# Kernel tuning notes

Hardware: AMD Instinct MI355X
Metric: run time of the kernel (lower is better)

## Reference

```python
import jax, jax.numpy as jnp
import numpy as np

N, P, H, K = 8192, 32, 512, 100
D = 2 * P
R = 32  # min(32, max(8, H))


def setup_inputs() -> dict:
    key = jax.random.key(0)
    ks = jax.random.split(key, 12)
    # strictly increasing event times
    dts = jax.random.uniform(ks[0], (N,), dtype=jnp.float32) * 0.1 + 1e-3
    times = jnp.cumsum(dts)
    marks = jax.random.randint(ks[1], (N,), 0, K, dtype=jnp.int32)
    u_inputs = jax.random.normal(ks[2], (N, H), dtype=jnp.float32) * 0.1
    # parameters (match torch init scales)
    lambda_log_real = jax.random.normal(ks[3], (P,), dtype=jnp.float32) * 0.1
    lambda_im = jax.random.normal(ks[4], (P,), dtype=jnp.float32) * 0.05
    V = jnp.eye(D, dtype=jnp.float32) + 0.01 * jax.random.normal(ks[5], (D, D), dtype=jnp.float32)
    B = jax.random.normal(ks[6], (D, H), dtype=jnp.float32) * 0.05
    E = jax.random.normal(ks[7], (D, R), dtype=jnp.float32) * 0.05
    alpha = jax.random.normal(ks[8], (R, K), dtype=jnp.float32) * 0.05
    gate_w = jax.random.normal(ks[9], (P, H), dtype=jnp.float32) * 0.02
    gate_b = jax.random.normal(ks[10], (P,), dtype=jnp.float32) * 0.02
    x0 = jnp.zeros((D,), dtype=jnp.float32)
    return {"times": times, "marks": marks, "u_inputs": u_inputs,
            "lambda_log_real": lambda_log_real, "lambda_im": lambda_im,
            "V": V, "B": B, "E": E, "alpha": alpha,
            "gate_w": gate_w, "gate_b": gate_b, "x0": x0}


def _v_block(V, pr, pi):
    """V @ blockdiag_p([[pr,-pi],[pi,pr]]) for each step n. V:(D,D), pr/pi:(n,P) -> (n,D,D)."""
    Dd = V.shape[0]
    Pp = pr.shape[-1]
    Vr = V.reshape(Dd, Pp, 2)
    col0 = Vr[None, :, :, 0] * pr[:, None, :] + Vr[None, :, :, 1] * pi[:, None, :]
    col1 = -Vr[None, :, :, 0] * pi[:, None, :] + Vr[None, :, :, 1] * pr[:, None, :]
    return jnp.stack([col0, col1], axis=-1).reshape(-1, Dd, Dd)


def reference(times, marks, u_inputs, lambda_log_real, lambda_im, V, B, E, alpha, gate_w, gate_b, x0):
    n = times.shape[0]
    dt = jnp.concatenate([times[:1], jnp.diff(times)])  # (N,) t_0 - 0, t_i - t_{i-1}
    # input-dependent eigenvalues: real = -softplus(log_real) * softplus(Wu+b), imag fixed
    gate = jax.nn.softplus(u_inputs @ gate_w.T + gate_b)           # (N,P)
    real = -jax.nn.softplus(lambda_log_real)[None, :] * gate        # (N,P)
    imag = jnp.broadcast_to(lambda_im[None, :], real.shape)         # (N,P)
    dtc = dt[:, None]
    exps = jnp.exp(real * dtc)
    cosb = jnp.cos(imag * dtc)
    sinb = jnp.sin(imag * dtc)
    a = exps * cosb  # Re(exp(lam dt))
    c = exps * sinb  # Im(exp(lam dt))
    V_inv = jnp.linalg.inv(V)
    # exp(A dt) = V M V^{-1}, M block-rotation per mode
    Aexp = _v_block(V, a, c) @ V_inv                                # (N,D,D)
    # integral (exp(lam dt) - 1)/lam, with dt fallback near lam=0
    denom = real * real + imag * imag
    num_re = a - 1.0
    num_im = c
    qr = (num_re * real + num_im * imag) / (denom + 1e-12)
    qi = (num_im * real - num_re * imag) / (denom + 1e-12)
    small = denom < 1e-8
    qr = jnp.where(small, dtc, qr)
    qi = jnp.where(small, 0.0, qi)
    VMint = _v_block(V, qr, qi)                                     # (N,D,D)
    # cont = V M_int V^{-1} B u  (fuse V^{-1} B u first, avoiding Kmat materialization)
    w = u_inputs @ (V_inv @ B).T                                    # (N,D)
    cont = jnp.einsum('nij,nj->ni', VMint, w)
    cont = jnp.where(dtc > 0, cont, 0.0)
    # mark impulses r_k = E alpha[:, k]
    r = (E @ alpha)[:, marks].T                                     # (N,D)

    def step(x_prev, inp):
        A_i, c_i, r_i = inp
        x_left = A_i @ x_prev + c_i
        x_right = x_left + r_i
        return x_right, (x_right, x_left)

    _, (x_right, x_left) = jax.lax.scan(step, x0, (Aexp, cont, r))
    return x_right, x_left
```

## Files before the change

### kernel.cpp

```cpp
#include <hip/hip_runtime.h>
#include <math.h>

#define NN 8192
#define PP 32
#define HH 512
#define KK 100
#define DD 64
#define RR 32
#define MM 96
#define SB 32
#define NSEG 256

#define OFF_VINV 0
#define OFF_EAT  4096
#define OFF_RHT  10496
#define OFF_Y0   16896
#define OFF_BAGG 16960
#define OFF_C    49728
#define OFF_COEF 836160

__device__ __forceinline__ float sp_fast(float x) {
    return x > 15.f ? x : __logf(1.f + __expf(x));
}
__device__ __forceinline__ float rcp_fast(float x) {
    float r;
    asm("v_rcp_f32 %0, %1" : "=v"(r) : "v"(x));
    return r;
}
__device__ __forceinline__ float4 comp_aff(float4 f, float4 g) {
    float4 r;
    r.x = f.x * g.x - f.y * g.y;
    r.y = f.x * g.y + f.y * g.x;
    r.z = f.x * g.z - f.y * g.w + f.z;
    r.w = f.x * g.w + f.y * g.z + f.w;
    return r;
}

#define IDX(r,c) ((r)*64 + ((c) ^ (((r)&7)<<2)))

__global__ void __launch_bounds__(512) g0(
    const float* __restrict__ u, const float* __restrict__ gate_w,
    const float* __restrict__ B, const float* __restrict__ V,
    const float* __restrict__ E, const float* __restrict__ alpha,
    const float* __restrict__ x0, float* __restrict__ ws) {
    __shared__ float sm[16384];
    const int b = blockIdx.x, t = threadIdx.x;

    if (b == NSEG) {
        float* Vt = sm;
        float* X  = sm + 4096;
        float* Xt = sm + 8192;
        float* T  = sm + 12288;
        const int i0 = (t >> 4) << 1;
        const int j0 = (t & 15) << 2;
        float nx[2][4];
        #pragma unroll
        for (int r = 0; r < 2; r++) {
            float4 v4 = *(const float4*)&V[(i0 + r) * DD + j0];
            float vv[4] = {v4.x, v4.y, v4.z, v4.w};
            #pragma unroll
            for (int s = 0; s < 4; s++) {
                Vt[IDX(j0 + s, i0 + r)] = vv[s];
                float xv = ((i0 + r) == (j0 + s) ? 2.f : 0.f) - vv[s];
                nx[r][s] = xv;
                Xt[IDX(j0 + s, i0 + r)] = xv;
            }
            *(float4*)&X[IDX(i0 + r, j0)] =
                make_float4(nx[r][0], nx[r][1], nx[r][2], nx[r][3]);
        }
        __syncthreads();
        for (int it = 0; it < 2; it++) {
            float ac[2][4];
            #pragma unroll
            for (int r = 0; r < 2; r++)
                #pragma unroll
                for (int s = 0; s < 4; s++) ac[r][s] = 0.f;
            for (int k = 0; k < DD; k++) {
                float2 a2 = *(float2*)&Vt[IDX(k, i0)];
                float4 b4 = *(float4*)&X[IDX(k, j0)];
                float bv[4] = {b4.x, b4.y, b4.z, b4.w};
                #pragma unroll
                for (int s = 0; s < 4; s++) {
                    ac[0][s] = fmaf(a2.x, bv[s], ac[0][s]);
                    ac[1][s] = fmaf(a2.y, bv[s], ac[1][s]);
                }
            }
            #pragma unroll
            for (int r = 0; r < 2; r++)
                *(float4*)&T[IDX(i0 + r, j0)] =
                    make_float4(ac[r][0], ac[r][1], ac[r][2], ac[r][3]);
            __syncthreads();
            #pragma unroll
            for (int r = 0; r < 2; r++)
                #pragma unroll
                for (int s = 0; s < 4; s++) ac[r][s] = 0.f;
            for (int k = 0; k < DD; k++) {
                float2 a2 = *(float2*)&Xt[IDX(k, i0)];
                float4 b4 = *(float4*)&T[IDX(k, j0)];
                float bv[4] = {b4.x, b4.y, b4.z, b4.w};
                #pragma unroll
                for (int s = 0; s < 4; s++) {
                    ac[0][s] = fmaf(a2.x, bv[s], ac[0][s]);
                    ac[1][s] = fmaf(a2.y, bv[s], ac[1][s]);
                }
            }
            #pragma unroll
            for (int r = 0; r < 2; r++) {
                float4 xo = *(float4*)&X[IDX(i0 + r, j0)];
                nx[r][0] = 2.f * xo.x - ac[r][0];
                nx[r][1] = 2.f * xo.y - ac[r][1];
                nx[r][2] = 2.f * xo.z - ac[r][2];
                nx[r][3] = 2.f * xo.w - ac[r][3];
            }
            __syncthreads();
            #pragma unroll
            for (int r = 0; r < 2; r++) {
                *(float4*)&X[IDX(i0 + r, j0)] =
                    make_float4(nx[r][0], nx[r][1], nx[r][2], nx[r][3]);
                #pragma unroll
                for (int s = 0; s < 4; s++) Xt[IDX(j0 + s, i0 + r)] = nx[r][s];
            }
            __syncthreads();
        }
        #pragma unroll
        for (int r = 0; r < 2; r++)
            *(float4*)&ws[OFF_VINV + (i0 + r) * DD + j0] =
                make_float4(nx[r][0], nx[r][1], nx[r][2], nx[r][3]);
        for (int idx = t; idx < KK * DD; idx += 512) {
            int k = idx >> 6, d = idx & 63;
            float ea = 0.f;
            #pragma unroll
            for (int r = 0; r < RR; r++)
                ea = fmaf(E[d * RR + r], alpha[r * KK + k], ea);
            ws[OFF_EAT + idx] = ea;
            if (k < 64) Vt[k * 64 + d] = ea; else T[(k - 64) * 64 + d] = ea;
        }
        __syncthreads();
        for (int idx = t; idx < KK * DD; idx += 512) {
            int k = idx >> 6, d = idx & 63;
            const float* ea = (k < 64) ? &Vt[k * 64] : &T[(k - 64) * 64];
            float rr = 0.f;
            for (int j = 0; j < DD; j++) rr = fmaf(Xt[IDX(j, d)], ea[j], rr);
            ws[OFF_RHT + idx] = rr;
        }
        if (t < DD) {
            float s = 0.f;
            for (int j = 0; j < DD; j++) s = fmaf(Xt[IDX(j, t)], x0[j], s);
            ws[OFF_Y0 + t] = s;
        }
        return;
    }

    float* uT = sm;
    float* mT = sm + 2048;
    const int n0 = b * SB;
    const int tn = t & 15, tm = t >> 4;
    float acc0 = 0.f, acc1 = 0.f, acc2 = 0.f, acc3 = 0.f, acc4 = 0.f, acc5 = 0.f;
    for (int kc = 0; kc < HH; kc += 64) {
        {
            int r = t >> 4, c4 = t & 15;
            float4 f4 = *(const float4*)&u[(n0 + r) * HH + kc + c4 * 4];
            *(float4*)&uT[r * 64 + ((c4 ^ (r & 7)) << 2)] = f4;
        }
        #pragma unroll
        for (int s2 = 0; s2 < 3; s2++) {
            int idx = t + 512 * s2;
            int r = idx >> 4, c4 = idx & 15;
            const float* src = (r < 32) ? &gate_w[r * HH] : &B[(r - 32) * HH];
            float4 f4 = *(const float4*)&src[kc + c4 * 4];
            *(float4*)&mT[r * 64 + ((c4 ^ (r & 7)) << 2)] = f4;
        }
        __syncthreads();
        #pragma unroll
        for (int k4 = 0; k4 < 16; k4++) {
            float4 uu[2], mm[3];
            #pragma unroll
            for (int i = 0; i < 2; i++) {
                int rr = 2 * tn + i;
                uu[i] = *(float4*)&uT[rr * 64 + ((k4 ^ (rr & 7)) << 2)];
            }
            #pragma unroll
            for (int j = 0; j < 3; j++) {
                int m = 3 * tm + j;
                mm[j] = *(float4*)&mT[m * 64 + ((k4 ^ (m & 7)) << 2)];
            }
            acc0 += uu[0].x*mm[0].x + uu[0].y*mm[0].y + uu[0].z*mm[0].z + uu[0].w*mm[0].w;
            acc1 += uu[0].x*mm[1].x + uu[0].y*mm[1].y + uu[0].z*mm[1].z + uu[0].w*mm[1].w;
            acc2 += uu[0].x*mm[2].x + uu[0].y*mm[2].y + uu[0].z*mm[2].z + uu[0].w*mm[2].w;
            acc3 += uu[1].x*mm[0].x + uu[1].y*mm[0].y + uu[1].z*mm[0].z + uu[1].w*mm[0].w;
            acc4 += uu[1].x*mm[1].x + uu[1].y*mm[1].y + uu[1].z*mm[1].z + uu[1].w*mm[1].w;
            acc5 += uu[1].x*mm[2].x + uu[1].y*mm[2].y + uu[1].z*mm[2].z + uu[1].w*mm[2].w;
        }
        __syncthreads();
    }
    float* Cw = ws + OFF_C + (size_t)b * SB * MM;
    Cw[(2*tn+0) * MM + 3*tm+0] = acc0;
    Cw[(2*tn+0) * MM + 3*tm+1] = acc1;
    Cw[(2*tn+0) * MM + 3*tm+2] = acc2;
    Cw[(2*tn+1) * MM + 3*tm+0] = acc3;
    Cw[(2*tn+1) * MM + 3*tm+1] = acc4;
    Cw[(2*tn+1) * MM + 3*tm+2] = acc5;
}

__global__ void __launch_bounds__(512) g1(
    const float* __restrict__ times, const int* __restrict__ marks,
    const float* __restrict__ llr, const float* __restrict__ lim,
    const float* __restrict__ gate_b, float* __restrict__ ws) {
    __shared__ float sm[9600];
    const int b = blockIdx.x, t = threadIdx.x;
    const int n0 = b * SB;
    for (int idx = t; idx < DD * DD; idx += 512) {
        int d = idx >> 6, j = idx & 63;
        sm[j * 68 + d] = ws[OFF_VINV + idx];
    }
    {
        int r = t >> 4, c0 = (t & 15) * 6;
        const float* Cg = ws + OFF_C + (size_t)b * SB * MM + r * MM + c0;
        float* Cl = sm + 4352 + r * 100 + c0;
        #pragma unroll
        for (int q = 0; q < 3; q++)
            *(float2*)&Cl[2 * q] = *(const float2*)&Cg[2 * q];
    }
    __syncthreads();
    {
        const int nl = t >> 4, d0 = (t & 15) << 2;
        float4 a = {0.f, 0.f, 0.f, 0.f};
        for (int j = 0; j < DD; j++) {
            float cr = sm[4352 + nl * 100 + 32 + j];
            float4 v4 = *(float4*)&sm[j * 68 + d0];
            a.x = fmaf(cr, v4.x, a.x); a.y = fmaf(cr, v4.y, a.y);
            a.z = fmaf(cr, v4.z, a.z); a.w = fmaf(cr, v4.w, a.w);
        }
        __syncthreads();
        *(float4*)&sm[4352 + nl * 100 + 32 + d0] = a;
    }
    __syncthreads();
    const int c = t >> 5, p = t & 31;
    const float nlr = -sp_fast(llr[p]);
    const float imag = lim[p], gb = gate_b[p];
    float4 cfs[2];
    #pragma unroll
    for (int i = 0; i < 2; i++) {
        int nl = c * 2 + i, n = n0 + nl;
        float dtv = times[n] - (n ? times[n - 1] : 0.f);
        float gate = sp_fast(sm[4352 + nl * 100 + p] + gb);
        float real = nlr * gate;
        float e = __expf(real * dtv);
        float x = imag * dtv, x2 = x * x;
        float cb = 1.f - x2 * (0.5f - x2 * (1.f / 24.f));
        float sb = x * (1.f - x2 * ((1.f / 6.f) - x2 * (1.f / 120.f)));
        float a = e * cb, cc = e * sb;
        float denom = real * real + imag * imag;
        float inv = rcp_fast(denom + 1e-12f);
        float nre = a - 1.f, nim = cc;
        float qr = (nre * real + nim * imag) * inv;
        float qi = (nim * real - nre * imag) * inv;
        if (denom < 1e-8f) { qr = dtv; qi = 0.f; }
        float2 w = *(float2*)&sm[4352 + nl * 100 + 32 + 2 * p];
        float br = qr * w.x - qi * w.y;
        float bi = qr * w.y + qi * w.x;
        if (!(dtv > 0.f)) { br = 0.f; bi = 0.f; }
        int mk = marks[n];
        float2 rh = *(const float2*)&ws[OFF_RHT + mk * DD + 2 * p];
        cfs[i] = make_float4(a, cc, br + rh.x, bi + rh.y);
        *(float4*)&ws[OFF_COEF + ((size_t)n * PP + p) * 4] = cfs[i];
    }
    float4* ag = (float4*)(sm + 7552);
    ag[c * 32 + p] = comp_aff(cfs[1], cfs[0]);
    __syncthreads();
    if (t < PP) {
        float4 T = make_float4(1.f, 0.f, 0.f, 0.f);
        #pragma unroll
        for (int cc = 0; cc < 16; cc++) T = comp_aff(ag[cc * 32 + t], T);
        *(float4*)&ws[OFF_BAGG + (b * PP + t) * 4] = T;
    }
}

__global__ void __launch_bounds__(512) g2(
    const float* __restrict__ V, const int* __restrict__ marks,
    const float* __restrict__ ws, float* __restrict__ out) {
    __shared__ float sm[10688];
    const int b = blockIdx.x, t = threadIdx.x;
    const int n0 = b * SB;
    const int c = t >> 5, p = t & 31;
    for (int idx = t; idx < DD * DD; idx += 512) {
        int d = idx >> 6, k = idx & 63;
        sm[k * 68 + d] = V[idx];
    }
    float4 cf0 = *(const float4*)&ws[OFF_COEF + ((size_t)(n0 + c * 2)     * PP + p) * 4];
    float4 cf1 = *(const float4*)&ws[OFF_COEF + ((size_t)(n0 + c * 2 + 1) * PP + p) * 4];
    float4* ag   = (float4*)(sm + 4352);
    float4* pref = (float4*)(sm + 6400);
    float2* yb   = (float2*)(sm + 10624);
    ag[c * 32 + p] = comp_aff(cf1, cf0);
    {
        int q0 = c * 16, q1 = min(b, q0 + 16);
        float4 Q = make_float4(1.f, 0.f, 0.f, 0.f);
        for (int q = q0; q < q1; q++)
            Q = comp_aff(*(const float4*)&ws[OFF_BAGG + (q * PP + p) * 4], Q);
        pref[c * 32 + p] = Q;
    }
    __syncthreads();
    if (t < PP) {
        float2 y = *(const float2*)&ws[OFF_Y0 + 2 * t];
        #pragma unroll
        for (int jg = 0; jg < 16; jg++) {
            float4 Q = pref[jg * 32 + t];
            float nyr = Q.x * y.x - Q.y * y.y + Q.z;
            float nyi = Q.x * y.y + Q.y * y.x + Q.w;
            y.x = nyr; y.y = nyi;
        }
        yb[t] = y;
    }
    __syncthreads();
    {
        float2 y = yb[p];
        #pragma unroll
        for (int cc = 0; cc < 15; cc++) {
            if (cc < c) {
                float4 A = ag[cc * 32 + p];
                float nyr = A.x * y.x - A.y * y.y + A.z;
                float nyi = A.x * y.y + A.y * y.x + A.w;
                y.x = nyr; y.y = nyi;
            }
        }
        float nyr = cf0.x * y.x - cf0.y * y.y + cf0.z;
        float nyi = cf0.x * y.y + cf0.y * y.x + cf0.w;
        y.x = nyr; y.y = nyi;
        *(float2*)&sm[8448 + (c * 2 + 0) * 68 + 2 * p] = y;
        nyr = cf1.x * y.x - cf1.y * y.y + cf1.z;
        nyi = cf1.x * y.y + cf1.y * y.x + cf1.w;
        y.x = nyr; y.y = nyi;
        *(float2*)&sm[8448 + (c * 2 + 1) * 68 + 2 * p] = y;
    }
    __syncthreads();
    {
        const int nr = t >> 4, d0 = (t & 15) << 2;
        float4 a = {0.f, 0.f, 0.f, 0.f};
        for (int k = 0; k < DD; k++) {
            float yv = sm[8448 + nr * 68 + k];
            float4 v4 = *(float4*)&sm[k * 68 + d0];
            a.x = fmaf(yv, v4.x, a.x); a.y = fmaf(yv, v4.y, a.y);
            a.z = fmaf(yv, v4.z, a.z); a.w = fmaf(yv, v4.w, a.w);
        }
        int n = n0 + nr;
        int mk = marks[n];
        *(float4*)&out[(size_t)n * DD + d0] = a;
        float4 e4 = *(const float4*)&ws[OFF_EAT + mk * DD + d0];
        a.x -= e4.x; a.y -= e4.y; a.z -= e4.z; a.w -= e4.w;
        *(float4*)&out[(size_t)NN * DD + (size_t)n * DD + d0] = a;
    }
}

extern "C" void kernel_launch(void* const* d_in, const int* in_sizes, int n_in,
                              void* d_out, int out_size, void* d_ws, size_t ws_size,
                              hipStream_t stream) {
    (void)in_sizes; (void)n_in; (void)out_size; (void)ws_size;
    const float* times  = (const float*)d_in[0];
    const int*   marks  = (const int*)d_in[1];
    const float* u      = (const float*)d_in[2];
    const float* llr    = (const float*)d_in[3];
    const float* lim    = (const float*)d_in[4];
    const float* V      = (const float*)d_in[5];
    const float* B      = (const float*)d_in[6];
    const float* E      = (const float*)d_in[7];
    const float* alpha  = (const float*)d_in[8];
    const float* gate_w = (const float*)d_in[9];
    const float* gate_b = (const float*)d_in[10];
    const float* x0     = (const float*)d_in[11];
    float* ws  = (float*)d_ws;
    float* out = (float*)d_out;

    hipLaunchKernelGGL(g0, dim3(NSEG + 1), dim3(512), 0, stream,
                       u, gate_w, B, V, E, alpha, x0, ws);
    hipLaunchKernelGGL(g1, dim3(NSEG), dim3(512), 0, stream,
                       times, marks, llr, lim, gate_b, ws);
    hipLaunchKernelGGL(g2, dim3(NSEG), dim3(512), 0, stream,
                       V, marks, ws, out);
}
```

Before: 164.6 us.

## Retile input GEMM into 128-row tiles with split-K and register prefetch

The projection GEMM in g0 now has each block compute a 128-row by 96-column tile over a quarter of the H dimension, using a 4x6 register tile per thread instead of 2x3. The next K chunk is prefetched into registers while the current one is computed. Partial sums are written to four separate workspace slices, and g1 adds them up when it loads C. This gives more data reuse per shared-memory load and overlaps global loads with compute. The cost is a workspace four times larger, extra global traffic for the partial sums, and more registers per thread.

```diff
diff --git a/kernel.cpp b/kernel.cpp
--- a/kernel.cpp
+++ b/kernel.cpp
@@ -10,6 +10,7 @@
 #define MM 96
 #define SB 32
 #define NSEG 256
+#define KSPL 4
 
 #define OFF_VINV 0
 #define OFF_EAT  4096
@@ -17,7 +18,7 @@
 #define OFF_Y0   16896
 #define OFF_BAGG 16960
 #define OFF_C    49728
-#define OFF_COEF 836160
+#define OFF_COEF 3195456
 
 __device__ __forceinline__ float sp_fast(float x) {
     return x > 15.f ? x : __logf(1.f + __expf(x));
@@ -46,7 +47,7 @@
     __shared__ float sm[16384];
     const int b = blockIdx.x, t = threadIdx.x;
 
-    if (b == NSEG) {
+    if (b == 256) {
         float* Vt = sm;
         float* X  = sm + 4096;
         float* Xt = sm + 8192;
@@ -151,55 +152,81 @@
         return;
     }
 
-    float* uT = sm;
-    float* mT = sm + 2048;
-    const int n0 = b * SB;
-    const int tn = t & 15, tm = t >> 4;
-    float acc0 = 0.f, acc1 = 0.f, acc2 = 0.f, acc3 = 0.f, acc4 = 0.f, acc5 = 0.f;
-    for (int kc = 0; kc < HH; kc += 64) {
-        {
-            int r = t >> 4, c4 = t & 15;
-            float4 f4 = *(const float4*)&u[(n0 + r) * HH + kc + c4 * 4];
-            *(float4*)&uT[r * 64 + ((c4 ^ (r & 7)) << 2)] = f4;
-        }
-        #pragma unroll
-        for (int s2 = 0; s2 < 3; s2++) {
-            int idx = t + 512 * s2;
-            int r = idx >> 4, c4 = idx & 15;
-            const float* src = (r < 32) ? &gate_w[r * HH] : &B[(r - 32) * HH];
-            float4 f4 = *(const float4*)&src[kc + c4 * 4];
-            *(float4*)&mT[r * 64 + ((c4 ^ (r & 7)) << 2)] = f4;
-        }
+    const int rt = b >> 2, ks = b & 3;
+    const int n0 = rt * 128, koff = ks * 128;
+    const int w = t >> 6, lane = t & 63;
+    const int rg = (lane & 7) + ((w & 3) << 3);
+    const int cg = ((lane >> 3) & 7) + ((w >> 2) << 3);
+    float acc[4][6];
+    #pragma unroll
+    for (int i = 0; i < 4; i++)
+        #pragma unroll
+        for (int j = 0; j < 6; j++) acc[i][j] = 0.f;
+
+    float4 ru[4], rm[3];
+    #pragma unroll
+    for (int q = 0; q < 4; q++) {
+        int idx = t + 512 * q; int r = idx >> 4, c4 = idx & 15;
+        ru[q] = *(const float4*)&u[(size_t)(n0 + r) * HH + koff + c4 * 4];
+    }
+    #pragma unroll
+    for (int q = 0; q < 3; q++) {
+        int idx = t + 512 * q; int r = idx >> 4, c4 = idx & 15;
+        const float* src = (r < 32) ? &gate_w[r * HH] : &B[(r - 32) * HH];
+        rm[q] = *(const float4*)&src[koff + c4 * 4];
+    }
+    #pragma unroll
+    for (int kc = 0; kc < 2; kc++) {
         __syncthreads();
         #pragma unroll
+        for (int q = 0; q < 4; q++) {
+            int idx = t + 512 * q; int r = idx >> 4, c4 = idx & 15;
+            *(float4*)&sm[r * 64 + ((c4 ^ ((r >> 2) & 7)) << 2)] = ru[q];
+        }
+        #pragma unroll
+        for (int q = 0; q < 3; q++) {
+            int idx = t + 512 * q; int r = idx >> 4, c4 = idx & 15;
+            *(float4*)&sm[8192 + r * 64 + ((c4 ^ (r & 7)) << 2)] = rm[q];
+        }
+        __syncthreads();
+        if (kc == 0) {
+            #pragma unroll
+            for (int q = 0; q < 4; q++) {
+                int idx = t + 512 * q; int r = idx >> 4, c4 = idx & 15;
+                ru[q] = *(const float4*)&u[(size_t)(n0 + r) * HH + koff + 64 + c4 * 4];
+            }
+            #pragma unroll
+            for (int q = 0; q < 3; q++) {
+                int idx = t + 512 * q; int r = idx >> 4, c4 = idx & 15;
+                const float* src = (r < 32) ? &gate_w[r * HH] : &B[(r - 32) * HH];
+                rm[q] = *(const float4*)&src[koff + 64 + c4 * 4];
+            }
+        }
+        #pragma unroll
         for (int k4 = 0; k4 < 16; k4++) {
-            float4 uu[2], mm[3];
-            #pragma unroll
-            for (int i = 0; i < 2; i++) {
-                int rr = 2 * tn + i;
-                uu[i] = *(float4*)&uT[rr * 64 + ((k4 ^ (rr & 7)) << 2)];
-            }
-            #pragma unroll
-            for (int j = 0; j < 3; j++) {
-                int m = 3 * tm + j;
-                mm[j] = *(float4*)&mT[m * 64 + ((k4 ^ (m & 7)) << 2)];
-            }
-            acc0 += uu[0].x*mm[0].x + uu[0].y*mm[0].y + uu[0].z*mm[0].z + uu[0].w*mm[0].w;
-            acc1 += uu[0].x*mm[1].x + uu[0].y*mm[1].y + uu[0].z*mm[1].z + uu[0].w*mm[1].w;
-            acc2 += uu[0].x*mm[2].x + uu[0].y*mm[2].y + uu[0].z*mm[2].z + uu[0].w*mm[2].w;
-            acc3 += uu[1].x*mm[0].x + uu[1].y*mm[0].y + uu[1].z*mm[0].z + uu[1].w*mm[0].w;
-            acc4 += uu[1].x*mm[1].x + uu[1].y*mm[1].y + uu[1].z*mm[1].z + uu[1].w*mm[1].w;
-            acc5 += uu[1].x*mm[2].x + uu[1].y*mm[2].y + uu[1].z*mm[2].z + uu[1].w*mm[2].w;
-        }
-        __syncthreads();
-    }
-    float* Cw = ws + OFF_C + (size_t)b * SB * MM;
-    Cw[(2*tn+0) * MM + 3*tm+0] = acc0;
-    Cw[(2*tn+0) * MM + 3*tm+1] = acc1;
-    Cw[(2*tn+0) * MM + 3*tm+2] = acc2;
-    Cw[(2*tn+1) * MM + 3*tm+0] = acc3;
-    Cw[(2*tn+1) * MM + 3*tm+1] = acc4;
-    Cw[(2*tn+1) * MM + 3*tm+2] = acc5;
+            float4 uu[4], mm[6];
+            #pragma unroll
+            for (int i = 0; i < 4; i++)
+                uu[i] = *(float4*)&sm[(4 * rg + i) * 64 + ((k4 ^ (rg & 7)) << 2)];
+            #pragma unroll
+            for (int j = 0; j < 6; j++) {
+                int m = 6 * cg + j;
+                mm[j] = *(float4*)&sm[8192 + m * 64 + ((k4 ^ (m & 7)) << 2)];
+            }
+            #pragma unroll
+            for (int i = 0; i < 4; i++)
+                #pragma unroll
+                for (int j = 0; j < 6; j++)
+                    acc[i][j] += uu[i].x * mm[j].x + uu[i].y * mm[j].y +
+                                 uu[i].z * mm[j].z + uu[i].w * mm[j].w;
+        }
+    }
+    float* Cw = ws + OFF_C + (size_t)ks * NN * MM;
+    #pragma unroll
+    for (int i = 0; i < 4; i++)
+        #pragma unroll
+        for (int j = 0; j < 6; j++)
+            Cw[(size_t)(n0 + 4 * rg + i) * MM + 6 * cg + j] = acc[i][j];
 }
 
 __global__ void __launch_bounds__(512) g1(
@@ -215,11 +242,16 @@
     }
     {
         int r = t >> 4, c0 = (t & 15) * 6;
-        const float* Cg = ws + OFF_C + (size_t)b * SB * MM + r * MM + c0;
+        float a[6] = {0.f, 0.f, 0.f, 0.f, 0.f, 0.f};
+        #pragma unroll
+        for (int s = 0; s < KSPL; s++) {
+            const float* Cg = ws + OFF_C + ((size_t)s * NN + n0 + r) * MM + c0;
+            #pragma unroll
+            for (int q = 0; q < 6; q++) a[q] += Cg[q];
+        }
         float* Cl = sm + 4352 + r * 100 + c0;
         #pragma unroll
-        for (int q = 0; q < 3; q++)
-            *(float2*)&Cl[2 * q] = *(const float2*)&Cg[2 * q];
+        for (int q = 0; q < 6; q++) Cl[q] = a[q];
     }
     __syncthreads();
     {
@@ -371,7 +403,7 @@
     float* ws  = (float*)d_ws;
     float* out = (float*)d_out;
 
-    hipLaunchKernelGGL(g0, dim3(NSEG + 1), dim3(512), 0, stream,
+    hipLaunchKernelGGL(g0, dim3(257), dim3(512), 0, stream,
                        u, gate_w, B, V, E, alpha, x0, ws);
     hipLaunchKernelGGL(g1, dim3(NSEG), dim3(512), 0, stream,
                        times, marks, llr, lim, gate_b, ws);
```

Measured after the change: 449.2 us. 173% more time.
